# Optimization experiments

Hardware: AMD Instinct MI355X
Metric: run time of the kernel (lower is better)

## Reference

```python
import jax, jax.numpy as jnp
import numpy as np

GRID = 7
COORD = 5.0
NO_OBJ = 0.5


def _corners(xywh, r, c):
    # xywh: [...,4] with (x_cell, y_cell, w, h); r,c broadcastable grid indices
    x, y, w, h = xywh[..., 0], xywh[..., 1], xywh[..., 2], xywh[..., 3]
    cx = (x + c) / GRID
    cy = (y + r) / GRID
    return cx - w / 2, cy - h / 2, cx + w / 2, cy + h / 2


def _iou(a, b):
    ax1, ay1, ax2, ay2 = a
    bx1, by1, bx2, by2 = b
    iw = jnp.maximum(jnp.minimum(ax2, bx2) - jnp.maximum(ax1, bx1), 0.0)
    ih = jnp.maximum(jnp.minimum(ay2, by2) - jnp.maximum(ay1, by1), 0.0)
    inter = iw * ih
    area_a = (ax2 - ax1) * (ay2 - ay1)
    area_b = (bx2 - bx1) * (by2 - by1)
    union = area_a + area_b - inter
    return jnp.where(union > 0, inter / jnp.where(union > 0, union, 1.0), 0.0)


def setup_inputs() -> dict:
    key = jax.random.key(0)
    k1, k2, k3 = jax.random.split(key, 3)
    B = 8192
    data = jax.random.uniform(k1, (B, GRID, GRID, 30), dtype=jnp.float32)
    labels = jax.random.uniform(k2, (B, GRID, GRID, 30), dtype=jnp.float32)
    # obj flag at channel 4 must be exactly 1 for obj cells
    obj = jax.random.randint(k3, (B, GRID, GRID), 0, 2).astype(jnp.float32)
    labels = labels.at[..., 4].set(obj)
    return {"data": data, "labels": labels}


def reference(data, labels):
    B = data.shape[0]
    r = jnp.arange(GRID, dtype=data.dtype)[None, :, None]  # row index -> y offset
    c = jnp.arange(GRID, dtype=data.dtype)[None, None, :]  # col index -> x offset

    box1 = _corners(data[..., 0:4], r, c)
    box2 = _corners(data[..., 5:9], r, c)
    gt = _corners(labels[..., 0:4], r, c)

    iou1 = _iou(box1, gt)  # [B,7,7]
    iou2 = _iou(box2, gt)
    resp1 = iou1 >= iou2

    xy1 = jnp.sum((data[..., 0:2] - labels[..., 0:2]) ** 2, -1)
    xy2 = jnp.sum((data[..., 5:7] - labels[..., 5:7]) ** 2, -1)
    wh1 = jnp.sum((jnp.sqrt(data[..., 2:4]) - jnp.sqrt(labels[..., 2:4])) ** 2, -1)
    wh2 = jnp.sum((jnp.sqrt(data[..., 7:9]) - jnp.sqrt(labels[..., 7:9])) ** 2, -1)

    d4, d9 = data[..., 4], data[..., 9]
    co = COORD * jnp.where(resp1, xy1, xy2)
    wh = COORD * jnp.where(resp1, wh1, wh2)
    confi = jnp.where(resp1, (d4 - iou1) ** 2, (d9 - iou2) ** 2)
    noobj_in = NO_OBJ * jnp.where(resp1, d9 ** 2, d4 ** 2)
    cls = jnp.sum((data[..., 10:] - labels[..., 10:]) ** 2, -1)

    m = (labels[..., 4] == 1).astype(data.dtype)
    obj_loss = m * (co + wh + confi + noobj_in + cls)
    noobj_loss = (1.0 - m) * NO_OBJ * (d4 ** 2 + d9 ** 2)
    return jnp.sum(obj_loss + noobj_loss) / B
```

## Files before the change

### kernel.cpp

```cpp
#include <hip/hip_runtime.h>

#define YGRID 7
#define COORD 5.0f
#define NO_OBJ 0.5f
#define NCELLS (8192 * 49)
#define INV_B (1.0f / 8192.0f)

__device__ __forceinline__ float iou_calc(float ax1, float ay1, float ax2, float ay2,
                                          float bx1, float by1, float bx2, float by2) {
    float iw = fminf(ax2, bx2) - fmaxf(ax1, bx1);
    iw = fmaxf(iw, 0.0f);
    float ih = fminf(ay2, by2) - fmaxf(ay1, by1);
    ih = fmaxf(ih, 0.0f);
    float inter = iw * ih;
    float area_a = (ax2 - ax1) * (ay2 - ay1);
    float area_b = (bx2 - bx1) * (by2 - by1);
    float uni = area_a + area_b - inter;
    return uni > 0.0f ? inter / uni : 0.0f;
}

__global__ __launch_bounds__(256) void yolo_loss_kernel(
    const float* __restrict__ data, const float* __restrict__ labels,
    float* __restrict__ out) {
    int idx = blockIdx.x * blockDim.x + threadIdx.x;

    float acc = 0.0f;
    if (idx < NCELLS) {
        int cell = idx % 49;
        float r = (float)(cell / 7);
        float c = (float)(cell % 7);

        const float2* dp = (const float2*)(data + (size_t)idx * 30);
        const float2* lp = (const float2*)(labels + (size_t)idx * 30);
        float d[30], l[30];
#pragma unroll
        for (int i = 0; i < 15; i++) {
            float2 v = dp[i];
            d[2 * i] = v.x; d[2 * i + 1] = v.y;
        }
#pragma unroll
        for (int i = 0; i < 15; i++) {
            float2 v = lp[i];
            l[2 * i] = v.x; l[2 * i + 1] = v.y;
        }

        const float inv_g = 1.0f / (float)YGRID;
        float cx1 = (d[0] + c) * inv_g, cy1 = (d[1] + r) * inv_g;
        float b1x1 = cx1 - d[2] * 0.5f, b1y1 = cy1 - d[3] * 0.5f;
        float b1x2 = cx1 + d[2] * 0.5f, b1y2 = cy1 + d[3] * 0.5f;
        float cx2 = (d[5] + c) * inv_g, cy2 = (d[6] + r) * inv_g;
        float b2x1 = cx2 - d[7] * 0.5f, b2y1 = cy2 - d[8] * 0.5f;
        float b2x2 = cx2 + d[7] * 0.5f, b2y2 = cy2 + d[8] * 0.5f;
        float gx = (l[0] + c) * inv_g, gy = (l[1] + r) * inv_g;
        float gx1 = gx - l[2] * 0.5f, gy1 = gy - l[3] * 0.5f;
        float gx2 = gx + l[2] * 0.5f, gy2 = gy + l[3] * 0.5f;

        float iou1 = iou_calc(b1x1, b1y1, b1x2, b1y2, gx1, gy1, gx2, gy2);
        float iou2 = iou_calc(b2x1, b2y1, b2x2, b2y2, gx1, gy1, gx2, gy2);
        bool resp1 = iou1 >= iou2;

        float xy1 = (d[0] - l[0]) * (d[0] - l[0]) + (d[1] - l[1]) * (d[1] - l[1]);
        float xy2 = (d[5] - l[5]) * (d[5] - l[5]) + (d[6] - l[6]) * (d[6] - l[6]);
        float s2 = sqrtf(d[2]) - sqrtf(l[2]);
        float s3 = sqrtf(d[3]) - sqrtf(l[3]);
        float wh1 = s2 * s2 + s3 * s3;
        float s7 = sqrtf(d[7]) - sqrtf(l[7]);
        float s8 = sqrtf(d[8]) - sqrtf(l[8]);
        float wh2 = s7 * s7 + s8 * s8;

        float d4 = d[4], d9 = d[9];
        float co = COORD * (resp1 ? xy1 : xy2);
        float wh = COORD * (resp1 ? wh1 : wh2);
        float ci = resp1 ? (d4 - iou1) * (d4 - iou1) : (d9 - iou2) * (d9 - iou2);
        float noobj_in = NO_OBJ * (resp1 ? d9 * d9 : d4 * d4);
        float cls = 0.0f;
#pragma unroll
        for (int i = 10; i < 30; i++) {
            float t = d[i] - l[i];
            cls += t * t;
        }

        float loss = (l[4] == 1.0f)
                         ? (co + wh + ci + noobj_in + cls)
                         : NO_OBJ * (d4 * d4 + d9 * d9);
        acc = loss * INV_B;
    }

#pragma unroll
    for (int off = 32; off > 0; off >>= 1)
        acc += __shfl_down(acc, off, 64);

    __shared__ float wsum[4];
    int lane = threadIdx.x & 63;
    int wid = threadIdx.x >> 6;
    if (lane == 0) wsum[wid] = acc;
    __syncthreads();
    if (threadIdx.x == 0) {
        float t = wsum[0] + wsum[1] + wsum[2] + wsum[3];
        atomicAdd(out, t);
    }
}

extern "C" void kernel_launch(void* const* d_in, const int* in_sizes, int n_in,
                              void* d_out, int out_size, void* d_ws, size_t ws_size,
                              hipStream_t stream) {
    const float* data = (const float*)d_in[0];
    const float* labels = (const float*)d_in[1];
    float* out = (float*)d_out;

    hipMemsetAsync(out, 0, sizeof(float) * out_size, stream);

    int nblocks = NCELLS / 256;
    yolo_loss_kernel<<<nblocks, 256, 0, stream>>>(data, labels, out);
}
```

Before: 135.1 us.

## Stage cell data through LDS with coalesced global_load_lds per wavefront

Each 64-thread block copies its contiguous 64 cells of data and labels into shared memory using direct global-to-LDS 16-byte loads. Threads then read their 30-float records from LDS, replacing per-thread strided global reads with fully coalesced ones. Blocks shrink to a single wavefront so the cross-wave shared reduction is dropped, at the cost of four times as many atomics and more blocks.

```diff
diff --git a/kernel.cpp b/kernel.cpp
--- a/kernel.cpp
+++ b/kernel.cpp
@@ -1,10 +1,15 @@
 #include <hip/hip_runtime.h>
 
-#define YGRID 7
 #define COORD 5.0f
 #define NO_OBJ 0.5f
 #define NCELLS (8192 * 49)
 #define INV_B (1.0f / 8192.0f)
+
+
+#define GLD(gaddr, laddr, sz)                                                        \
+    __builtin_amdgcn_global_load_lds(                                                \
+        (const __attribute__((address_space(1))) void*)(gaddr),                      \
+        (__attribute__((address_space(3))) void*)(laddr), (sz), 0, 0)
 
 __device__ __forceinline__ float iou_calc(float ax1, float ay1, float ax2, float ay2,
                                           float bx1, float by1, float bx2, float by2) {
@@ -19,86 +24,92 @@
     return uni > 0.0f ? inter / uni : 0.0f;
 }
 
-__global__ __launch_bounds__(256) void yolo_loss_kernel(
+__global__ __launch_bounds__(64) void yolo_loss_kernel(
     const float* __restrict__ data, const float* __restrict__ labels,
     float* __restrict__ out) {
-    int idx = blockIdx.x * blockDim.x + threadIdx.x;
+    __shared__ float sd[1920];
+    __shared__ float sl[1920];
 
-    float acc = 0.0f;
-    if (idx < NCELLS) {
-        int cell = idx % 49;
-        float r = (float)(cell / 7);
-        float c = (float)(cell % 7);
+    const int ln = threadIdx.x;
+    const size_t fbase = (size_t)blockIdx.x * 1920;
 
-        const float2* dp = (const float2*)(data + (size_t)idx * 30);
-        const float2* lp = (const float2*)(labels + (size_t)idx * 30);
-        float d[30], l[30];
+    const float4* gd4 = (const float4*)(data + fbase);
+    const float4* gl4 = (const float4*)(labels + fbase);
+    float4* sd4 = (float4*)sd;
+    float4* sl4 = (float4*)sl;
 #pragma unroll
-        for (int i = 0; i < 15; i++) {
-            float2 v = dp[i];
-            d[2 * i] = v.x; d[2 * i + 1] = v.y;
-        }
+    for (int j = 0; j < 7; j++) {
+        GLD(gd4 + j * 64 + ln, sd4 + j * 64 + ln, 16);
+        GLD(gl4 + j * 64 + ln, sl4 + j * 64 + ln, 16);
+    }
 #pragma unroll
-        for (int i = 0; i < 15; i++) {
-            float2 v = lp[i];
-            l[2 * i] = v.x; l[2 * i + 1] = v.y;
-        }
+    for (int k = 0; k < 2; k++) {
+        GLD(data + fbase + 1792 + k * 64 + ln, sd + 1792 + k * 64 + ln, 4);
+        GLD(labels + fbase + 1792 + k * 64 + ln, sl + 1792 + k * 64 + ln, 4);
+    }
+    __syncthreads();
 
-        const float inv_g = 1.0f / (float)YGRID;
-        float cx1 = (d[0] + c) * inv_g, cy1 = (d[1] + r) * inv_g;
-        float b1x1 = cx1 - d[2] * 0.5f, b1y1 = cy1 - d[3] * 0.5f;
-        float b1x2 = cx1 + d[2] * 0.5f, b1y2 = cy1 + d[3] * 0.5f;
-        float cx2 = (d[5] + c) * inv_g, cy2 = (d[6] + r) * inv_g;
-        float b2x1 = cx2 - d[7] * 0.5f, b2y1 = cy2 - d[8] * 0.5f;
-        float b2x2 = cx2 + d[7] * 0.5f, b2y2 = cy2 + d[8] * 0.5f;
-        float gx = (l[0] + c) * inv_g, gy = (l[1] + r) * inv_g;
-        float gx1 = gx - l[2] * 0.5f, gy1 = gy - l[3] * 0.5f;
-        float gx2 = gx + l[2] * 0.5f, gy2 = gy + l[3] * 0.5f;
+    const int idx = blockIdx.x * 64 + ln;
+    const int cell = idx % 49;
+    const float r = (float)(cell / 7);
+    const float c = (float)(cell % 7);
 
-        float iou1 = iou_calc(b1x1, b1y1, b1x2, b1y2, gx1, gy1, gx2, gy2);
-        float iou2 = iou_calc(b2x1, b2y1, b2x2, b2y2, gx1, gy1, gx2, gy2);
-        bool resp1 = iou1 >= iou2;
+    float d[30], l[30];
+    const float2* dp = (const float2*)(sd + ln * 30);
+    const float2* lp = (const float2*)(sl + ln * 30);
+#pragma unroll
+    for (int i = 0; i < 15; i++) {
+        float2 v = dp[i];
+        d[2 * i] = v.x; d[2 * i + 1] = v.y;
+        float2 w2 = lp[i];
+        l[2 * i] = w2.x; l[2 * i + 1] = w2.y;
+    }
 
-        float xy1 = (d[0] - l[0]) * (d[0] - l[0]) + (d[1] - l[1]) * (d[1] - l[1]);
-        float xy2 = (d[5] - l[5]) * (d[5] - l[5]) + (d[6] - l[6]) * (d[6] - l[6]);
-        float s2 = sqrtf(d[2]) - sqrtf(l[2]);
-        float s3 = sqrtf(d[3]) - sqrtf(l[3]);
-        float wh1 = s2 * s2 + s3 * s3;
-        float s7 = sqrtf(d[7]) - sqrtf(l[7]);
-        float s8 = sqrtf(d[8]) - sqrtf(l[8]);
-        float wh2 = s7 * s7 + s8 * s8;
+    const float inv_g = 1.0f / 7.0f;
+    float cx1 = (d[0] + c) * inv_g, cy1 = (d[1] + r) * inv_g;
+    float b1x1 = cx1 - d[2] * 0.5f, b1y1 = cy1 - d[3] * 0.5f;
+    float b1x2 = cx1 + d[2] * 0.5f, b1y2 = cy1 + d[3] * 0.5f;
+    float cx2 = (d[5] + c) * inv_g, cy2 = (d[6] + r) * inv_g;
+    float b2x1 = cx2 - d[7] * 0.5f, b2y1 = cy2 - d[8] * 0.5f;
+    float b2x2 = cx2 + d[7] * 0.5f, b2y2 = cy2 + d[8] * 0.5f;
+    float gx = (l[0] + c) * inv_g, gy = (l[1] + r) * inv_g;
+    float gx1 = gx - l[2] * 0.5f, gy1 = gy - l[3] * 0.5f;
+    float gx2 = gx + l[2] * 0.5f, gy2 = gy + l[3] * 0.5f;
 
-        float d4 = d[4], d9 = d[9];
-        float co = COORD * (resp1 ? xy1 : xy2);
-        float wh = COORD * (resp1 ? wh1 : wh2);
-        float ci = resp1 ? (d4 - iou1) * (d4 - iou1) : (d9 - iou2) * (d9 - iou2);
-        float noobj_in = NO_OBJ * (resp1 ? d9 * d9 : d4 * d4);
-        float cls = 0.0f;
+    float iou1 = iou_calc(b1x1, b1y1, b1x2, b1y2, gx1, gy1, gx2, gy2);
+    float iou2 = iou_calc(b2x1, b2y1, b2x2, b2y2, gx1, gy1, gx2, gy2);
+    bool resp1 = iou1 >= iou2;
+
+    float xy1 = (d[0] - l[0]) * (d[0] - l[0]) + (d[1] - l[1]) * (d[1] - l[1]);
+    float xy2 = (d[5] - l[5]) * (d[5] - l[5]) + (d[6] - l[6]) * (d[6] - l[6]);
+    float s2 = sqrtf(d[2]) - sqrtf(l[2]);
+    float s3 = sqrtf(d[3]) - sqrtf(l[3]);
+    float wh1 = s2 * s2 + s3 * s3;
+    float s7 = sqrtf(d[7]) - sqrtf(l[7]);
+    float s8 = sqrtf(d[8]) - sqrtf(l[8]);
+    float wh2 = s7 * s7 + s8 * s8;
+
+    float d4 = d[4], d9 = d[9];
+    float co = COORD * (resp1 ? xy1 : xy2);
+    float wh = COORD * (resp1 ? wh1 : wh2);
+    float ci = resp1 ? (d4 - iou1) * (d4 - iou1) : (d9 - iou2) * (d9 - iou2);
+    float noobj_in = NO_OBJ * (resp1 ? d9 * d9 : d4 * d4);
+    float cls = 0.0f;
 #pragma unroll
-        for (int i = 10; i < 30; i++) {
-            float t = d[i] - l[i];
-            cls += t * t;
-        }
+    for (int i = 10; i < 30; i++) {
+        float t = d[i] - l[i];
+        cls += t * t;
+    }
 
-        float loss = (l[4] == 1.0f)
-                         ? (co + wh + ci + noobj_in + cls)
-                         : NO_OBJ * (d4 * d4 + d9 * d9);
-        acc = loss * INV_B;
-    }
+    float loss = (l[4] == 1.0f)
+                     ? (co + wh + ci + noobj_in + cls)
+                     : NO_OBJ * (d4 * d4 + d9 * d9);
+    float acc = loss * INV_B;
 
 #pragma unroll
     for (int off = 32; off > 0; off >>= 1)
         acc += __shfl_down(acc, off, 64);
-
-    __shared__ float wsum[4];
-    int lane = threadIdx.x & 63;
-    int wid = threadIdx.x >> 6;
-    if (lane == 0) wsum[wid] = acc;
-    __syncthreads();
-    if (threadIdx.x == 0) {
-        float t = wsum[0] + wsum[1] + wsum[2] + wsum[3];
-        atomicAdd(out, t);
-    }
+    if (ln == 0) atomicAdd(out, acc);
 }
 
 extern "C" void kernel_launch(void* const* d_in, const int* in_sizes, int n_in,
@@ -110,6 +121,6 @@
 
     hipMemsetAsync(out, 0, sizeof(float) * out_size, stream);
 
-    int nblocks = NCELLS / 256;
-    yolo_loss_kernel<<<nblocks, 256, 0, stream>>>(data, labels, out);
+    int nblocks = NCELLS / 64;
+    yolo_loss_kernel<<<nblocks, 64, 0, stream>>>(data, labels, out);
 }
```

After: 176.7 us. 1.31x slower.
